# Optimization experiments

Hardware: AMD Instinct MI355X
Metric: run time of the kernel (lower is better)

## Reference

```python
import jax, jax.numpy as jnp
import numpy as np

D_MODEL = 1024
N_HEAD = 16
D_HEAD = D_MODEL // N_HEAD
D_FF = 4096
EPS = 1e-5


def _layernorm(x, gamma, beta):
    mu = jnp.mean(x, axis=-1, keepdims=True)
    var = jnp.mean(jnp.square(x - mu), axis=-1, keepdims=True)
    return (x - mu) * jax.lax.rsqrt(var + EPS) * gamma + beta


def setup_inputs() -> dict:
    key = jax.random.key(0)
    ks = jax.random.split(key, 16)
    s = 1.0 / np.sqrt(D_MODEL)
    sf = 1.0 / np.sqrt(D_FF)
    return {
        "src": jax.random.normal(ks[0], (8, 1024, D_MODEL), dtype=jnp.float32),
        "Wq": jax.random.uniform(ks[1], (D_MODEL, D_MODEL), jnp.float32, -s, s),
        "bq": jnp.zeros((D_MODEL,), jnp.float32),
        "Wk": jax.random.uniform(ks[2], (D_MODEL, D_MODEL), jnp.float32, -s, s),
        "bk": jnp.zeros((D_MODEL,), jnp.float32),
        "Wv": jax.random.uniform(ks[3], (D_MODEL, D_MODEL), jnp.float32, -s, s),
        "bv": jnp.zeros((D_MODEL,), jnp.float32),
        "Wo": jax.random.uniform(ks[4], (D_MODEL, D_MODEL), jnp.float32, -s, s),
        "bo": jnp.zeros((D_MODEL,), jnp.float32),
        "W1": jax.random.uniform(ks[5], (D_MODEL, D_FF), jnp.float32, -s, s),
        "b1": jnp.zeros((D_FF,), jnp.float32),
        "W2": jax.random.uniform(ks[6], (D_FF, D_MODEL), jnp.float32, -sf, sf),
        "b2": jnp.zeros((D_MODEL,), jnp.float32),
        "g1": jnp.ones((D_MODEL,), jnp.float32),
        "beta1": jnp.zeros((D_MODEL,), jnp.float32),
        "g2": jnp.ones((D_MODEL,), jnp.float32),
        "beta2": jnp.zeros((D_MODEL,), jnp.float32),
    }


def reference(src, Wq, bq, Wk, bk, Wv, bv, Wo, bo, W1, b1, W2, b2, g1, beta1, g2, beta2):
    B, S, _ = src.shape
    x = _layernorm(src, g1, beta1)
    # QKV projections -> [B, H, S, Dh]
    def split_heads(t):
        return t.reshape(B, S, N_HEAD, D_HEAD).transpose(0, 2, 1, 3)
    q = split_heads(x @ Wq + bq)
    k = split_heads(x @ Wk + bk)
    v = split_heads(x @ Wv + bv)
    # SymbolicAttention (canonical graph): softmax(q k^T / sqrt(d_head)) v
    scores = jnp.einsum('bhqd,bhkd->bhqk', q, k) / np.sqrt(D_HEAD).astype(np.float32)
    attn = jax.nn.softmax(scores, axis=-1)
    ctx = jnp.einsum('bhqk,bhkd->bhqd', attn, v)
    ctx = ctx.transpose(0, 2, 1, 3).reshape(B, S, D_MODEL)
    src = src + (ctx @ Wo + bo)  # dropout is identity in eval
    y = _layernorm(src, g2, beta2)
    ffn = jax.nn.relu(y @ W1 + b1) @ W2 + b2
    return src + ffn
```

## Files before the change

### kernel.cpp

```cpp
#include <hip/hip_runtime.h>
#include <stdint.h>

#define D_MODEL 1024
#define N_HEAD  16
#define D_HEAD  64
#define D_FF    4096
#define SEQ     1024
#define BATCH   8
#define M_TOK   (BATCH*SEQ)

typedef __attribute__((ext_vector_type(8))) short bf16x8;
typedef __attribute__((ext_vector_type(4))) float f32x4;

__device__ __forceinline__ float bf2f(unsigned short u) {
    union { unsigned int u; float f; } x; x.u = ((unsigned int)u) << 16; return x.f;
}
__device__ __forceinline__ unsigned short f2bf(float f) {
    union { float f; unsigned int u; } x; x.f = f;
    unsigned int r = x.u + 0x7fffu + ((x.u >> 16) & 1u);
    return (unsigned short)(r >> 16);
}

typedef const __attribute__((address_space(1))) unsigned int* gas_t;
typedef __attribute__((address_space(3))) unsigned int* las_t;
__device__ __forceinline__ void gl_lds16(const unsigned short* g, unsigned short* l) {
    __builtin_amdgcn_global_load_lds((gas_t)g, (las_t)l, 16, 0, 0);
}

#define DSR(dst, addr, IMM) \
    asm volatile("ds_read_b128 %0, %1 offset:" #IMM : "=v"(dst) : "v"(addr))

#define SBAR()  asm volatile("s_barrier")
#define SB0()   __builtin_amdgcn_sched_barrier(0)
#define WAITL0() asm volatile("s_waitcnt lgkmcnt(0)")
#define WAITV6() asm volatile("s_waitcnt vmcnt(6)")
#define WAITV2() asm volatile("s_waitcnt vmcnt(2)")
#define WAITV0() asm volatile("s_waitcnt vmcnt(0)")

__global__ __launch_bounds__(256) void transpose_cvt(
        const float* __restrict__ src, unsigned short* __restrict__ dst,
        int R, int C)
{
    __shared__ float t[32][33];
    const int tx = threadIdx.x & 31, ty = threadIdx.x >> 5;
    const int c0 = blockIdx.x * 32, r0 = blockIdx.y * 32;
    #pragma unroll
    for (int i = 0; i < 32; i += 8)
        t[ty + i][tx] = src[(size_t)(r0 + ty + i) * C + c0 + tx];
    __syncthreads();
    #pragma unroll
    for (int i = 0; i < 32; i += 8)
        dst[(size_t)(c0 + ty + i) * R + r0 + tx] = f2bf(t[tx][ty + i]);
}

__global__ __launch_bounds__(256) void ln_kernel(
        const float* __restrict__ x, const float* __restrict__ g,
        const float* __restrict__ be, unsigned short* __restrict__ out)
{
    const int row = blockIdx.x, tid = threadIdx.x;
    const f32x4 v = *(const f32x4*)(x + (size_t)row * D_MODEL + tid * 4);
    float s  = v[0] + v[1] + v[2] + v[3];
    float ss = v[0]*v[0] + v[1]*v[1] + v[2]*v[2] + v[3]*v[3];
    #pragma unroll
    for (int o = 1; o < 64; o <<= 1) { s += __shfl_xor(s, o); ss += __shfl_xor(ss, o); }
    __shared__ float sa[4], sb[4];
    const int wv = tid >> 6;
    if ((tid & 63) == 0) { sa[wv] = s; sb[wv] = ss; }
    __syncthreads();
    s  = sa[0] + sa[1] + sa[2] + sa[3];
    ss = sb[0] + sb[1] + sb[2] + sb[3];
    const float mu   = s * (1.0f / D_MODEL);
    const float rstd = rsqrtf(ss * (1.0f / D_MODEL) - mu * mu + 1e-5f);
    const f32x4 gv = *(const f32x4*)(g  + tid * 4);
    const f32x4 bv = *(const f32x4*)(be + tid * 4);
    unsigned short w[4];
    #pragma unroll
    for (int j = 0; j < 4; j++) w[j] = f2bf((v[j] - mu) * rstd * gv[j] + bv[j]);
    *(uint2*)(out + (size_t)row * D_MODEL + tid * 4) = *(uint2*)w;
}

template<int MODE>
__global__ __launch_bounds__(512, 2) void gemm256(
        const unsigned short* __restrict__ A,
        const unsigned short* __restrict__ BT,
        const float* __restrict__ b1_,
        const float* __restrict__ b2_,
        const float* __restrict__ b3_,
        void* __restrict__ Cout,
        int M, int N, int K)
{
    (void)M;
    __shared__ unsigned short As[32768];
    __shared__ unsigned short Bs[32768];

    const int tid  = threadIdx.x;
    const int wave = tid >> 6, lane = tid & 63;
    const int quad = lane >> 4, l16 = lane & 15;
    const int wm = wave >> 2, wn = wave & 3;

    const int nbx = gridDim.x;
    const int bid = blockIdx.x + nbx * blockIdx.y;
    const int chunk = (nbx * gridDim.y) >> 3;
    const int lg = (bid & 7) * chunk + (bid >> 3);
    const int m0 = (lg / nbx) * 256;
    const int n0 = (lg % nbx) * 256;
    const int NT = K >> 6;

    const int st_row = tid >> 3;
    const int st_g   = (tid & 7) ^ (st_row & 7);
    const unsigned short* gA = A  + (size_t)(m0 + st_row) * K + st_g * 8;
    const unsigned short* gB = BT + (size_t)(n0 + st_row) * K + st_g * 8;
    unsigned short* lA = As + wave * 512;
    unsigned short* lB = Bs + wave * 512;

    const unsigned asBase = (unsigned)(size_t)(las_t)(void*)As;
    const unsigned bsBase = (unsigned)(size_t)(las_t)(void*)Bs;
    const unsigned aOff = (unsigned)((wm * 64 + l16) * 128);
    const unsigned bOff = (unsigned)((wn * 32 + l16) * 128);
    const unsigned s0b  = (unsigned)((quad ^ (l16 & 7)) * 16);
    const unsigned s1b  = s0b ^ 64;

    f32x4 acc[8][4] = {};

#define STAGE_A(T, H, D) \
    do { gl_lds16(gA + (size_t)((H)*128   )*K + (size_t)(T)*64, lA + (D)*16384 + (H)*8192); \
         gl_lds16(gA + (size_t)((H)*128+64)*K + (size_t)(T)*64, lA + (D)*16384 + (H)*8192 + 4096); } while(0)
#define STAGE_B(T, H, D) \
    do { gl_lds16(gB + (size_t)((H)*128   )*K + (size_t)(T)*64, lB + (D)*16384 + (H)*8192); \
         gl_lds16(gB + (size_t)((H)*128+64)*K + (size_t)(T)*64, lB + (D)*16384 + (H)*8192 + 4096); } while(0)

    STAGE_A(0, 0, 0); STAGE_B(0, 0, 0); STAGE_B(0, 1, 0); STAGE_A(0, 1, 0);
    STAGE_A(1, 0, 1); STAGE_B(1, 0, 1); STAGE_B(1, 1, 1);
    SB0(); WAITV6();
    SBAR(); SB0();

    for (int t = 0; t < NT; ++t) {
        const int db = t & 1;
        const unsigned dbo = (unsigned)(db * 32768);
        const unsigned aR0 = asBase + dbo + aOff + s0b;
        const unsigned aR1 = asBase + dbo + aOff + s1b;
        const unsigned bR0 = bsBase + dbo + bOff + s0b;
        const unsigned bR1 = bsBase + dbo + bOff + s1b;
        bf16x8 a0[4], a1[4], bA0[2], bA1[2], bB0[2], bB1[2];

        DSR(a0[0], aR0, 0);    DSR(a0[1], aR0, 2048);
        DSR(a0[2], aR0, 4096); DSR(a0[3], aR0, 6144);
        DSR(a1[0], aR1, 0);    DSR(a1[1], aR1, 2048);
        DSR(a1[2], aR1, 4096); DSR(a1[3], aR1, 6144);
        DSR(bA0[0], bR0, 0);   DSR(bA0[1], bR0, 2048);
        DSR(bA1[0], bR1, 0);   DSR(bA1[1], bR1, 2048);
        if (t + 1 < NT) STAGE_A(t + 1, 1, db ^ 1);
        SB0(); SBAR(); SB0();
        WAITL0(); SB0();
        __builtin_amdgcn_s_setprio(1);
        #pragma unroll
        for (int mi = 0; mi < 4; ++mi)
            #pragma unroll
            for (int ni = 0; ni < 2; ++ni)
                acc[mi][ni] = __builtin_amdgcn_mfma_f32_16x16x32_bf16(
                        bA0[ni], a0[mi], acc[mi][ni], 0, 0, 0);
        #pragma unroll
        for (int mi = 0; mi < 4; ++mi)
            #pragma unroll
            for (int ni = 0; ni < 2; ++ni)
                acc[mi][ni] = __builtin_amdgcn_mfma_f32_16x16x32_bf16(
                        bA1[ni], a1[mi], acc[mi][ni], 0, 0, 0);
        __builtin_amdgcn_s_setprio(0);
        SB0(); SBAR(); SB0();

        DSR(bB0[0], bR0, 16384);   DSR(bB0[1], bR0, 18432);
        DSR(bB1[0], bR1, 16384);   DSR(bB1[1], bR1, 18432);
        if (t + 2 < NT) STAGE_A(t + 2, 0, db);
        SB0(); SBAR(); SB0();
        WAITL0(); SB0();
        __builtin_amdgcn_s_setprio(1);
        #pragma unroll
        for (int mi = 0; mi < 4; ++mi)
            #pragma unroll
            for (int ni = 0; ni < 2; ++ni)
                acc[mi][2 + ni] = __builtin_amdgcn_mfma_f32_16x16x32_bf16(
                        bB0[ni], a0[mi], acc[mi][2 + ni], 0, 0, 0);
        #pragma unroll
        for (int mi = 0; mi < 4; ++mi)
            #pragma unroll
            for (int ni = 0; ni < 2; ++ni)
                acc[mi][2 + ni] = __builtin_amdgcn_mfma_f32_16x16x32_bf16(
                        bB1[ni], a1[mi], acc[mi][2 + ni], 0, 0, 0);
        __builtin_amdgcn_s_setprio(0);
        SB0(); SBAR(); SB0();

        DSR(a0[0], aR0, 16384); DSR(a0[1], aR0, 18432);
        DSR(a0[2], aR0, 20480); DSR(a0[3], aR0, 22528);
        DSR(a1[0], aR1, 16384); DSR(a1[1], aR1, 18432);
        DSR(a1[2], aR1, 20480); DSR(a1[3], aR1, 22528);
        if (t + 2 < NT) STAGE_B(t + 2, 0, db);
        SB0(); SBAR(); SB0();
        WAITL0(); SB0();
        __builtin_amdgcn_s_setprio(1);
        #pragma unroll
        for (int mi = 0; mi < 4; ++mi)
            #pragma unroll
            for (int ni = 0; ni < 2; ++ni)
                acc[4 + mi][ni] = __builtin_amdgcn_mfma_f32_16x16x32_bf16(
                        bA0[ni], a0[mi], acc[4 + mi][ni], 0, 0, 0);
        #pragma unroll
        for (int mi = 0; mi < 4; ++mi)
            #pragma unroll
            for (int ni = 0; ni < 2; ++ni)
                acc[4 + mi][ni] = __builtin_amdgcn_mfma_f32_16x16x32_bf16(
                        bA1[ni], a1[mi], acc[4 + mi][ni], 0, 0, 0);
        __builtin_amdgcn_s_setprio(0);
        SB0(); SBAR(); SB0();

        if (t + 2 < NT) { STAGE_B(t + 2, 1, db); SB0(); WAITV6(); }
        else            { SB0(); WAITV0(); }
        SBAR(); SB0();
        __builtin_amdgcn_s_setprio(1);
        #pragma unroll
        for (int mi = 0; mi < 4; ++mi)
            #pragma unroll
            for (int ni = 0; ni < 2; ++ni)
                acc[4 + mi][2 + ni] = __builtin_amdgcn_mfma_f32_16x16x32_bf16(
                        bB0[ni], a0[mi], acc[4 + mi][2 + ni], 0, 0, 0);
        #pragma unroll
        for (int mi = 0; mi < 4; ++mi)
            #pragma unroll
            for (int ni = 0; ni < 2; ++ni)
                acc[4 + mi][2 + ni] = __builtin_amdgcn_mfma_f32_16x16x32_bf16(
                        bB1[ni], a1[mi], acc[4 + mi][2 + ni], 0, 0, 0);
        __builtin_amdgcn_s_setprio(0);
        SB0(); SBAR(); SB0();
    }
#undef STAGE_A
#undef STAGE_B

    if (MODE == 1) {
        unsigned short* dst = (unsigned short*)Cout;
        #pragma unroll
        for (int f = 0; f < 8; ++f) {
            const int row = m0 + (f >> 2) * 128 + wm * 64 + (f & 3) * 16 + l16;
            #pragma unroll
            for (int g = 0; g < 4; ++g) {
                const int col = n0 + (g >> 1) * 128 + wn * 32 + (g & 1) * 16 + quad * 4;
                const f32x4 bs4 = *(const f32x4*)(b1_ + col);
                unsigned short w[4];
                #pragma unroll
                for (int r = 0; r < 4; ++r)
                    w[r] = f2bf(fmaxf(acc[f][g][r] + bs4[r], 0.0f));
                *(uint2*)(dst + (size_t)row * N + col) = *(uint2*)w;
            }
        }
    } else {
        const int rt = n0 >> 10;
        if (rt < 2) {
            unsigned short* dst = (unsigned short*)Cout + (size_t)rt * M_TOK * 1024;
            const float sc = (rt == 0) ? 0.125f : 1.0f;
            const float* bs = (rt == 0) ? b1_ : b2_;
            const int nb = n0 & 1023;
            #pragma unroll
            for (int f = 0; f < 8; ++f) {
                const int row = m0 + (f >> 2) * 128 + wm * 64 + (f & 3) * 16 + l16;
                #pragma unroll
                for (int g = 0; g < 4; ++g) {
                    const int col = nb + (g >> 1) * 128 + wn * 32 + (g & 1) * 16 + quad * 4;
                    const f32x4 bs4 = *(const f32x4*)(bs + col);
                    unsigned short w[4];
                    #pragma unroll
                    for (int r = 0; r < 4; ++r)
                        w[r] = f2bf((acc[f][g][r] + bs4[r]) * sc);
                    *(uint2*)(dst + (size_t)row * 1024 + col) = *(uint2*)w;
                }
            }
        } else {
            unsigned short* vdst = (unsigned short*)Cout + (size_t)2 * M_TOK * 1024;
            const int nb = n0 - 2048;
            #pragma unroll
            for (int f = 0; f < 8; ++f) {
                const int row = m0 + (f >> 2) * 128 + wm * 64 + (f & 3) * 16 + l16;
                const int bb = row >> 10, s = row & 1023;
                #pragma unroll
                for (int g = 0; g < 4; ++g) {
                    const int cc = nb + (g >> 1) * 128 + wn * 32 + (g & 1) * 16 + quad * 4;
                    #pragma unroll
                    for (int r = 0; r < 4; ++r)
                        vdst[((size_t)(bb * 1024 + cc + r)) * 1024 + s]
                            = f2bf(acc[f][g][r] + b3_[cc + r]);
                }
            }
        }
    }
}

__global__ __launch_bounds__(512, 2) void gemm_n128(
        const unsigned short* __restrict__ A,
        const unsigned short* __restrict__ BT,
        const float* __restrict__ bias,
        const float* __restrict__ resid,
        float* __restrict__ Cout,
        int N, int K)
{
    __shared__ unsigned short As[32768];
    __shared__ unsigned short Bs[16384];

    const int tid  = threadIdx.x;
    const int wave = tid >> 6, lane = tid & 63;
    const int quad = lane >> 4, l16 = lane & 15;
    const int wm = wave >> 1, wn = wave & 1;

    const int nbx = gridDim.x;
    const int bid = blockIdx.x + nbx * blockIdx.y;
    const int chunk = (nbx * gridDim.y) >> 3;
    const int lg = (bid & 7) * chunk + (bid >> 3);
    const int m0 = (lg / nbx) * 256;
    const int n0 = (lg % nbx) * 128;
    const int NT = K >> 6;

    const int st_row = tid >> 3;
    const int st_g   = (tid & 7) ^ (st_row & 7);
    const unsigned short* gA = A  + (size_t)(m0 + st_row) * K + st_g * 8;
    const unsigned short* gB = BT + (size_t)(n0 + st_row) * K + st_g * 8;
    unsigned short* lA = As + wave * 512;
    unsigned short* lB = Bs + wave * 512;

    const unsigned asBase = (unsigned)(size_t)(las_t)(void*)As;
    const unsigned bsBase = (unsigned)(size_t)(las_t)(void*)Bs;
    const unsigned aOff = (unsigned)((wm * 32 + l16) * 128);
    const unsigned bOff = (unsigned)((wn * 64 + l16) * 128);
    const unsigned s0b  = (unsigned)((quad ^ (l16 & 7)) * 16);
    const unsigned s1b  = s0b ^ 64;

    f32x4 acc[4][4] = {};

#define STG_A(T, H, D) \
    do { gl_lds16(gA + (size_t)((H)*128   )*K + (size_t)(T)*64, lA + (D)*16384 + (H)*8192); \
         gl_lds16(gA + (size_t)((H)*128+64)*K + (size_t)(T)*64, lA + (D)*16384 + (H)*8192 + 4096); } while(0)
#define STG_B(T, D) \
    do { gl_lds16(gB + (size_t)(T)*64,                 lB + (D)*8192); \
         gl_lds16(gB + (size_t)64*K + (size_t)(T)*64,  lB + (D)*8192 + 4096); } while(0)

    STG_A(0, 0, 0); STG_B(0, 0); STG_A(0, 1, 0);
    STG_A(1, 0, 1); STG_B(1, 1);
    SB0(); WAITV6();
    SBAR(); SB0();

    for (int t = 0; t < NT; ++t) {
        const int db = t & 1;
        const unsigned aR0 = asBase + (unsigned)(db << 15) + aOff + s0b;
        const unsigned aR1 = asBase + (unsigned)(db << 15) + aOff + s1b;
        const unsigned bR0 = bsBase + (unsigned)(db << 14) + bOff + s0b;
        const unsigned bR1 = bsBase + (unsigned)(db << 14) + bOff + s1b;
        bf16x8 a0[2][2], a1[2][2], bf[4][2];

        DSR(a0[0][0], aR0, 0);    DSR(a0[1][0], aR0, 2048);
        DSR(a0[0][1], aR1, 0);    DSR(a0[1][1], aR1, 2048);
        DSR(bf[0][0], bR0, 0);    DSR(bf[1][0], bR0, 2048);
        DSR(bf[2][0], bR0, 4096); DSR(bf[3][0], bR0, 6144);
        DSR(bf[0][1], bR1, 0);    DSR(bf[1][1], bR1, 2048);
        DSR(bf[2][1], bR1, 4096); DSR(bf[3][1], bR1, 6144);
        if (t + 1 < NT) STG_A(t + 1, 1, db ^ 1);
        SB0(); SBAR(); SB0();
        WAITL0(); SB0();
        __builtin_amdgcn_s_setprio(1);
        #pragma unroll
        for (int mi = 0; mi < 2; ++mi)
            #pragma unroll
            for (int ni = 0; ni < 4; ++ni)
                acc[mi][ni] = __builtin_amdgcn_mfma_f32_16x16x32_bf16(
                        bf[ni][0], a0[mi][0], acc[mi][ni], 0, 0, 0);
        #pragma unroll
        for (int mi = 0; mi < 2; ++mi)
            #pragma unroll
            for (int ni = 0; ni < 4; ++ni)
                acc[mi][ni] = __builtin_amdgcn_mfma_f32_16x16x32_bf16(
                        bf[ni][1], a0[mi][1], acc[mi][ni], 0, 0, 0);
        __builtin_amdgcn_s_setprio(0);
        SB0();
        if (t + 1 < NT) WAITV6(); else WAITV0();
        SBAR(); SB0();

        DSR(a1[0][0], aR0, 16384); DSR(a1[1][0], aR0, 18432);
        DSR(a1[0][1], aR1, 16384); DSR(a1[1][1], aR1, 18432);
        if (t + 2 < NT) { STG_A(t + 2, 0, db); STG_B(t + 2, db); }
        SB0(); SBAR(); SB0();
        WAITL0(); SB0();
        __builtin_amdgcn_s_setprio(1);
        #pragma unroll
        for (int mi = 0; mi < 2; ++mi)
            #pragma unroll
            for (int ni = 0; ni < 4; ++ni)
                acc[2 + mi][ni] = __builtin_amdgcn_mfma_f32_16x16x32_bf16(
                        bf[ni][0], a1[mi][0], acc[2 + mi][ni], 0, 0, 0);
        #pragma unroll
        for (int mi = 0; mi < 2; ++mi)
            #pragma unroll
            for (int ni = 0; ni < 4; ++ni)
                acc[2 + mi][ni] = __builtin_amdgcn_mfma_f32_16x16x32_bf16(
                        bf[ni][1], a1[mi][1], acc[2 + mi][ni], 0, 0, 0);
        __builtin_amdgcn_s_setprio(0);
        SB0();
        if (t + 2 < NT)      { WAITV6(); SBAR(); }
        else if (t + 1 < NT) { WAITV2(); SBAR(); }
        SB0();
    }
#undef STG_A
#undef STG_B

    #pragma unroll
    for (int qm = 0; qm < 2; ++qm)
        #pragma unroll
        for (int mi = 0; mi < 2; ++mi) {
            const int row = m0 + qm * 128 + wm * 32 + mi * 16 + l16;
            #pragma unroll
            for (int ni = 0; ni < 4; ++ni) {
                const int col = n0 + wn * 64 + ni * 16 + quad * 4;
                const f32x4 bs4 = *(const f32x4*)(bias + col);
                const f32x4 rv  = *(const f32x4*)(resid + (size_t)row * N + col);
                f32x4 o;
                #pragma unroll
                for (int r = 0; r < 4; ++r)
                    o[r] = acc[qm * 2 + mi][ni][r] + bs4[r] + rv[r];
                *(f32x4*)(Cout + (size_t)row * N + col) = o;
            }
        }
}

#define ASTR 72
__global__ __launch_bounds__(256) void attn_mfma(
        const unsigned short* __restrict__ Q,
        const unsigned short* __restrict__ K,
        const unsigned short* __restrict__ VT,
        unsigned short* __restrict__ CTX)
{
    __shared__ unsigned short Ks[64 * ASTR];
    __shared__ unsigned short Vs[64 * ASTR];
    __shared__ unsigned short Ps[128 * ASTR];

    const int tid  = threadIdx.x;
    const int wave = tid >> 6, lane = tid & 63;
    const int quad = lane >> 4, l16 = lane & 15;
    const int bh = blockIdx.y;
    const int q0 = blockIdx.x * 128;
    const size_t baseQ = (size_t)(bh >> 4) * SEQ * D_MODEL + (size_t)(bh & 15) * D_HEAD;
    const size_t baseV = (size_t)bh * D_HEAD * SEQ;
    const int strip = wave * 32;

    bf16x8 qf[2][2];
    #pragma unroll
    for (int mt = 0; mt < 2; mt++)
        #pragma unroll
        for (int h = 0; h < 2; h++)
            qf[mt][h] = *(const bf16x8*)(Q + baseQ
                        + (size_t)(q0 + strip + mt * 16 + l16) * D_MODEL
                        + h * 32 + quad * 8);

    f32x4 of[2][4] = {};
    float l_p[2][4] = {};

    for (int c = 0; c < SEQ / 64; c++) {
        const int k0 = c * 64;
        __syncthreads();
        #pragma unroll
        for (int u = tid; u < 512; u += 256) {
            const int r = u >> 3, g = (u & 7) * 8;
            *(uint4*)(Ks + r * ASTR + g) =
                *(const uint4*)(K + baseQ + (size_t)(k0 + r) * D_MODEL + g);
            *(uint4*)(Vs + r * ASTR + g) =
                *(const uint4*)(VT + baseV + (size_t)r * SEQ + k0 + g);
        }
        __syncthreads();

        bf16x8 kf[4][2];
        #pragma unroll
        for (int kt = 0; kt < 4; kt++)
            #pragma unroll
            for (int h = 0; h < 2; h++)
                kf[kt][h] = *(const bf16x8*)(Ks + (kt * 16 + l16) * ASTR + h * 32 + quad * 8);

        #pragma unroll
        for (int mt = 0; mt < 2; mt++) {
            f32x4 s[4] = {};
            #pragma unroll
            for (int h = 0; h < 2; h++)
                #pragma unroll
                for (int kt = 0; kt < 4; kt++)
                    s[kt] = __builtin_amdgcn_mfma_f32_16x16x32_bf16(
                            qf[mt][h], kf[kt][h], s[kt], 0, 0, 0);
            #pragma unroll
            for (int kt = 0; kt < 4; kt++)
                #pragma unroll
                for (int r = 0; r < 4; r++) {
                    const float p = __expf(s[kt][r]);
                    l_p[mt][r] += p;
                    Ps[(strip + mt * 16 + quad * 4 + r) * ASTR + kt * 16 + l16] = f2bf(p);
                }
        }

        bf16x8 pf[2][2];
        #pragma unroll
        for (int mt = 0; mt < 2; mt++)
            #pragma unroll
            for (int h = 0; h < 2; h++)
                pf[mt][h] = *(const bf16x8*)(Ps + (strip + mt * 16 + l16) * ASTR
                                             + h * 32 + quad * 8);
        #pragma unroll
        for (int nt = 0; nt < 4; nt++) {
            bf16x8 vf[2];
            #pragma unroll
            for (int h = 0; h < 2; h++)
                vf[h] = *(const bf16x8*)(Vs + (nt * 16 + l16) * ASTR + h * 32 + quad * 8);
            #pragma unroll
            for (int mt = 0; mt < 2; mt++)
                #pragma unroll
                for (int h = 0; h < 2; h++)
                    of[mt][nt] = __builtin_amdgcn_mfma_f32_16x16x32_bf16(
                            pf[mt][h], vf[h], of[mt][nt], 0, 0, 0);
        }
    }

    #pragma unroll
    for (int mt = 0; mt < 2; mt++) {
        float inv[4];
        #pragma unroll
        for (int r = 0; r < 4; r++) {
            float l = l_p[mt][r];
            #pragma unroll
            for (int o = 1; o < 16; o <<= 1) l += __shfl_xor(l, o);
            inv[r] = 1.0f / l;
        }
        #pragma unroll
        for (int nt = 0; nt < 4; nt++)
            #pragma unroll
            for (int r = 0; r < 4; r++)
                CTX[baseQ + (size_t)(q0 + strip + mt * 16 + quad * 4 + r) * D_MODEL
                    + nt * 16 + l16] = f2bf(of[mt][nt][r] * inv[r]);
    }
}

extern "C" void kernel_launch(void* const* d_in, const int* in_sizes, int n_in,
                              void* d_out, int out_size, void* d_ws, size_t ws_size,
                              hipStream_t stream)
{
    (void)in_sizes; (void)n_in; (void)out_size; (void)ws_size;
    const float* src = (const float*)d_in[0];
    const float* Wq  = (const float*)d_in[1];
    const float* bq  = (const float*)d_in[2];
    const float* Wk  = (const float*)d_in[3];
    const float* bk  = (const float*)d_in[4];
    const float* Wv  = (const float*)d_in[5];
    const float* bv  = (const float*)d_in[6];
    const float* Wo  = (const float*)d_in[7];
    const float* bo  = (const float*)d_in[8];
    const float* W1  = (const float*)d_in[9];
    const float* b1  = (const float*)d_in[10];
    const float* W2  = (const float*)d_in[11];
    const float* b2  = (const float*)d_in[12];
    const float* g1  = (const float*)d_in[13];
    const float* be1 = (const float*)d_in[14];
    const float* g2  = (const float*)d_in[15];
    const float* be2 = (const float*)d_in[16];
    float* out = (float*)d_out;

    unsigned short* wqkvT = (unsigned short*)d_ws;
    unsigned short* woT = wqkvT + (size_t)3 * 1024 * 1024;
    unsigned short* w1T = woT + 1024 * 1024;
    unsigned short* w2T = w1T + (size_t)4096 * 1024;
    unsigned short* xn  = w2T + (size_t)1024 * 4096;
    unsigned short* q   = xn  + (size_t)M_TOK * D_MODEL;
    unsigned short* k   = q   + (size_t)M_TOK * D_MODEL;
    unsigned short* vT  = k   + (size_t)M_TOK * D_MODEL;
    unsigned short* ctx = vT  + (size_t)M_TOK * D_MODEL;
    unsigned short* hid = ctx + (size_t)M_TOK * D_MODEL;

    const dim3 blk(256);
    const dim3 blk512(512);

    transpose_cvt<<<dim3(32, 32),  blk, 0, stream>>>(Wq, wqkvT,                 1024, 1024);
    transpose_cvt<<<dim3(32, 32),  blk, 0, stream>>>(Wk, wqkvT + 1024 * 1024,   1024, 1024);
    transpose_cvt<<<dim3(32, 32),  blk, 0, stream>>>(Wv, wqkvT + 2 * 1024 * 1024, 1024, 1024);
    transpose_cvt<<<dim3(32, 32),  blk, 0, stream>>>(Wo, woT, 1024, 1024);
    transpose_cvt<<<dim3(128, 32), blk, 0, stream>>>(W1, w1T, 1024, 4096);
    transpose_cvt<<<dim3(32, 128), blk, 0, stream>>>(W2, w2T, 4096, 1024);

    ln_kernel<<<M_TOK, blk, 0, stream>>>(src, g1, be1, xn);

    gemm256<3><<<dim3(12, 32), blk512, 0, stream>>>(
        xn, wqkvT, bq, bk, bv, q, M_TOK, 3072, D_MODEL);

    attn_mfma<<<dim3(SEQ / 128, BATCH * N_HEAD), blk, 0, stream>>>(q, k, vT, ctx);

    gemm_n128<<<dim3(8, 32), blk512, 0, stream>>>(
        ctx, woT, bo, src, out, D_MODEL, D_MODEL);

    ln_kernel<<<M_TOK, blk, 0, stream>>>(out, g2, be2, xn);

    gemm256<1><<<dim3(16, 32), blk512, 0, stream>>>(
        xn, w1T, b1, nullptr, nullptr, hid, M_TOK, D_FF, D_MODEL);

    gemm_n128<<<dim3(8, 32), blk512, 0, stream>>>(
        hid, w2T, b2, out, out, D_MODEL, D_FF);
}
```

Before: 498.8 us.

## Merge barriers in GEMM mainloops and defer global-to-LDS wait counts

Restructures the synchronisation in both bf16 GEMM main loops. The post-MFMA barriers are removed, and each phase now waits on a finer vmcnt, hits one barrier, then issues the next global_load_lds prefetch. This roughly halves the barriers per iteration and keeps more async loads in flight. The cost is more delicate wait-count bookkeeping, where a wrong count could race on the LDS buffers.

Result: no change. 490.2 us (-1.7%).

```diff
diff --git a/kernel.cpp b/kernel.cpp
--- a/kernel.cpp
+++ b/kernel.cpp
@@ -30,12 +30,10 @@
 #define DSR(dst, addr, IMM) \
     asm volatile("ds_read_b128 %0, %1 offset:" #IMM : "=v"(dst) : "v"(addr))
 
-#define SBAR()  asm volatile("s_barrier")
-#define SB0()   __builtin_amdgcn_sched_barrier(0)
+#define SBAR()   asm volatile("s_barrier")
+#define SB0()    __builtin_amdgcn_sched_barrier(0)
 #define WAITL0() asm volatile("s_waitcnt lgkmcnt(0)")
-#define WAITV6() asm volatile("s_waitcnt vmcnt(6)")
-#define WAITV2() asm volatile("s_waitcnt vmcnt(2)")
-#define WAITV0() asm volatile("s_waitcnt vmcnt(0)")
+#define WAITV(N) asm volatile("s_waitcnt vmcnt(" #N ")")
 
 __global__ __launch_bounds__(256) void transpose_cvt(
         const float* __restrict__ src, unsigned short* __restrict__ dst,
@@ -131,7 +129,7 @@
 
     STAGE_A(0, 0, 0); STAGE_B(0, 0, 0); STAGE_B(0, 1, 0); STAGE_A(0, 1, 0);
     STAGE_A(1, 0, 1); STAGE_B(1, 0, 1); STAGE_B(1, 1, 1);
-    SB0(); WAITV6();
+    SB0(); WAITV(10);
     SBAR(); SB0();
 
     for (int t = 0; t < NT; ++t) {
@@ -149,9 +147,10 @@
         DSR(a1[2], aR1, 4096); DSR(a1[3], aR1, 6144);
         DSR(bA0[0], bR0, 0);   DSR(bA0[1], bR0, 2048);
         DSR(bA1[0], bR1, 0);   DSR(bA1[1], bR1, 2048);
+        if (t + 1 < NT) WAITV(8); else WAITV(2);
+        SBAR(); SB0();
+        WAITL0(); SB0();
         if (t + 1 < NT) STAGE_A(t + 1, 1, db ^ 1);
-        SB0(); SBAR(); SB0();
-        WAITL0(); SB0();
         __builtin_amdgcn_s_setprio(1);
         #pragma unroll
         for (int mi = 0; mi < 4; ++mi)
@@ -166,13 +165,14 @@
                 acc[mi][ni] = __builtin_amdgcn_mfma_f32_16x16x32_bf16(
                         bA1[ni], a1[mi], acc[mi][ni], 0, 0, 0);
         __builtin_amdgcn_s_setprio(0);
-        SB0(); SBAR(); SB0();
+        SB0();
 
         DSR(bB0[0], bR0, 16384);   DSR(bB0[1], bR0, 18432);
         DSR(bB1[0], bR1, 16384);   DSR(bB1[1], bR1, 18432);
+        if (t + 1 < NT) WAITV(8); else WAITV(0);
+        SBAR(); SB0();
+        WAITL0(); SB0();
         if (t + 2 < NT) STAGE_A(t + 2, 0, db);
-        SB0(); SBAR(); SB0();
-        WAITL0(); SB0();
         __builtin_amdgcn_s_setprio(1);
         #pragma unroll
         for (int mi = 0; mi < 4; ++mi)
@@ -187,15 +187,15 @@
                 acc[mi][2 + ni] = __builtin_amdgcn_mfma_f32_16x16x32_bf16(
                         bB1[ni], a1[mi], acc[mi][2 + ni], 0, 0, 0);
         __builtin_amdgcn_s_setprio(0);
-        SB0(); SBAR(); SB0();
+        SB0();
 
         DSR(a0[0], aR0, 16384); DSR(a0[1], aR0, 18432);
         DSR(a0[2], aR0, 20480); DSR(a0[3], aR0, 22528);
         DSR(a1[0], aR1, 16384); DSR(a1[1], aR1, 18432);
         DSR(a1[2], aR1, 20480); DSR(a1[3], aR1, 22528);
+        SBAR(); SB0();
+        WAITL0(); SB0();
         if (t + 2 < NT) STAGE_B(t + 2, 0, db);
-        SB0(); SBAR(); SB0();
-        WAITL0(); SB0();
         __builtin_amdgcn_s_setprio(1);
         #pragma unroll
         for (int mi = 0; mi < 4; ++mi)
@@ -210,11 +210,13 @@
                 acc[4 + mi][ni] = __builtin_amdgcn_mfma_f32_16x16x32_bf16(
                         bA1[ni], a1[mi], acc[4 + mi][ni], 0, 0, 0);
         __builtin_amdgcn_s_setprio(0);
-        SB0(); SBAR(); SB0();
-
-        if (t + 2 < NT) { STAGE_B(t + 2, 1, db); SB0(); WAITV6(); }
-        else            { SB0(); WAITV0(); }
+        SB0();
+
+        if (t + 2 < NT)      WAITV(8);
+        else if (t + 1 < NT) WAITV(4);
+        else                 WAITV(0);
         SBAR(); SB0();
+        if (t + 2 < NT) STAGE_B(t + 2, 1, db);
         __builtin_amdgcn_s_setprio(1);
         #pragma unroll
         for (int mi = 0; mi < 4; ++mi)
@@ -229,8 +231,9 @@
                 acc[4 + mi][2 + ni] = __builtin_amdgcn_mfma_f32_16x16x32_bf16(
                         bB1[ni], a1[mi], acc[4 + mi][2 + ni], 0, 0, 0);
         __builtin_amdgcn_s_setprio(0);
-        SB0(); SBAR(); SB0();
+        SB0();
     }
+    WAITV(0); SB0();
 #undef STAGE_A
 #undef STAGE_B
 
@@ -340,7 +343,7 @@
 
     STG_A(0, 0, 0); STG_B(0, 0); STG_A(0, 1, 0);
     STG_A(1, 0, 1); STG_B(1, 1);
-    SB0(); WAITV6();
+    SB0(); WAITV(6);
     SBAR(); SB0();
 
     for (int t = 0; t < NT; ++t) {
@@ -357,9 +360,10 @@
         DSR(bf[2][0], bR0, 4096); DSR(bf[3][0], bR0, 6144);
         DSR(bf[0][1], bR1, 0);    DSR(bf[1][1], bR1, 2048);
         DSR(bf[2][1], bR1, 4096); DSR(bf[3][1], bR1, 6144);
+        if (t + 1 < NT) WAITV(4); else WAITV(0);
+        SBAR(); SB0();
+        WAITL0(); SB0();
         if (t + 1 < NT) STG_A(t + 1, 1, db ^ 1);
-        SB0(); SBAR(); SB0();
-        WAITL0(); SB0();
         __builtin_amdgcn_s_setprio(1);
         #pragma unroll
         for (int mi = 0; mi < 2; ++mi)
@@ -375,14 +379,13 @@
                         bf[ni][1], a0[mi][1], acc[mi][ni], 0, 0, 0);
         __builtin_amdgcn_s_setprio(0);
         SB0();
-        if (t + 1 < NT) WAITV6(); else WAITV0();
-        SBAR(); SB0();
 
         DSR(a1[0][0], aR0, 16384); DSR(a1[1][0], aR0, 18432);
         DSR(a1[0][1], aR1, 16384); DSR(a1[1][1], aR1, 18432);
+        if (t + 1 < NT) WAITV(2); else WAITV(0);
+        SBAR(); SB0();
+        WAITL0(); SB0();
         if (t + 2 < NT) { STG_A(t + 2, 0, db); STG_B(t + 2, db); }
-        SB0(); SBAR(); SB0();
-        WAITL0(); SB0();
         __builtin_amdgcn_s_setprio(1);
         #pragma unroll
         for (int mi = 0; mi < 2; ++mi)
@@ -398,10 +401,8 @@
                         bf[ni][1], a1[mi][1], acc[2 + mi][ni], 0, 0, 0);
         __builtin_amdgcn_s_setprio(0);
         SB0();
-        if (t + 2 < NT)      { WAITV6(); SBAR(); }
-        else if (t + 1 < NT) { WAITV2(); SBAR(); }
-        SB0();
     }
+    WAITV(0); SB0();
 #undef STG_A
 #undef STG_B
 
```
